# Performance work log

Hardware: AMD Instinct MI355X
Metric: run time of the kernel (lower is better)

## Reference

```python
import jax, jax.numpy as jnp
import numpy as np

N = 50000        # nodes
E = 1_600_000    # edges
F_IN = 128       # in_channels
H = 128          # hidden_dim (== F_IN so GCN weights stack)
L = 3            # num_layers
LSTM_H = 256     # lstm_hidden
OUT = 32         # output_dim
G = 64           # number of graphs in the batch


def setup_inputs() -> dict:
    key = jax.random.key(0)
    ks = jax.random.split(key, 8)
    x = jax.random.normal(ks[0], (N, F_IN), dtype=jnp.float32)
    edge_index = jax.random.randint(ks[1], (2, E), 0, N, dtype=jnp.int32)
    batch = jnp.sort(jax.random.randint(ks[2], (N,), 0, G, dtype=jnp.int32))
    # GCN layer weights (all [H,H] since F_IN == H), PyG-style glorot scale
    Wg = jax.random.normal(ks[3], (L, F_IN, H), dtype=jnp.float32) / np.sqrt(F_IN)
    bg = jnp.zeros((L, H), dtype=jnp.float32)
    # torch LSTM params, gate order (i, f, g, o)
    W_ih = jax.random.normal(ks[4], (4 * LSTM_H, H), dtype=jnp.float32) / np.sqrt(H)
    W_hh = jax.random.normal(ks[5], (4 * LSTM_H, LSTM_H), dtype=jnp.float32) / np.sqrt(LSTM_H)
    b_ih = jnp.zeros((4 * LSTM_H,), dtype=jnp.float32)
    b_hh = jnp.zeros((4 * LSTM_H,), dtype=jnp.float32)
    W_out = jax.random.normal(ks[6], (OUT, LSTM_H), dtype=jnp.float32) / np.sqrt(LSTM_H)
    b_out = jnp.zeros((OUT,), dtype=jnp.float32)
    return dict(x=x, edge_index=edge_index, batch=batch, Wg=Wg, bg=bg,
                W_ih=W_ih, W_hh=W_hh, b_ih=b_ih, b_hh=b_hh,
                W_out=W_out, b_out=b_out)


def reference(x, edge_index, batch, Wg, bg, W_ih, W_hh, b_ih, b_hh, W_out, b_out):
    n = x.shape[0]
    # PyG GCNConv gcn_norm: add self-loops, symmetric D^{-1/2}(A+I)D^{-1/2}
    loop = jnp.arange(n, dtype=edge_index.dtype)
    row = jnp.concatenate([edge_index[0], loop])  # source nodes (x_j)
    col = jnp.concatenate([edge_index[1], loop])  # target nodes (aggregate here)
    deg = jax.ops.segment_sum(jnp.ones_like(col, dtype=x.dtype), col, num_segments=n)
    dinv = jnp.where(deg > 0, jax.lax.rsqrt(deg), 0.0)
    norm = (dinv[row] * dinv[col])[:, None]  # [E+N, 1]

    h = x
    for l in range(Wg.shape[0]):
        t = h @ Wg[l]                                     # [N, H] transform first
        msg = t[row] * norm                               # gather + scale  [E+N, H]
        agg = jax.ops.segment_sum(msg, col, num_segments=n)  # scatter-add  [N, H]
        h = jax.nn.relu(agg + bg[l])

    # global_mean_pool over batch segment ids
    cnt = jax.ops.segment_sum(jnp.ones((n,), h.dtype), batch, num_segments=G)
    pooled = jax.ops.segment_sum(h, batch, num_segments=G) / jnp.maximum(cnt, 1.0)[:, None]  # [G, H]

    # single-step LSTM with zero initial state (seq_len = 1)
    h0 = jnp.zeros((G, W_hh.shape[1]), pooled.dtype)
    gates = pooled @ W_ih.T + h0 @ W_hh.T + b_ih + b_hh   # [G, 4*LSTM_H]
    i, f, g, o = jnp.split(gates, 4, axis=-1)             # torch gate order i,f,g,o
    c = jax.nn.sigmoid(i) * jnp.tanh(g)                   # c0 = 0 => forget term drops
    hn = jax.nn.sigmoid(o) * jnp.tanh(c)                  # [G, LSTM_H]

    return hn @ W_out.T + b_out                            # [G, OUT]
```

## Files before the change

kernel.cpp:

```cpp
#include <hip/hip_runtime.h>

constexpr int NN = 50000;
constexpr int NE = 1600000;
constexpr int H  = 128;
constexpr int LH = 256;
constexpr int OD = 32;
constexpr int NG = 64;

constexpr int NBKT  = (NN + 255) / 256;
constexpr int PARTE = 4096;
constexpr int NPARTB = (NE + PARTE - 1) / PARTE;
static_assert(NBKT <= 256, "single-block scan assumes NBKT <= 256");

constexpr int NCH = 8;
constexpr int CHW = 16;
constexpr int BCH = 4;
constexpr int BCW = 32;

constexpr int LSZ = 4608;

typedef __attribute__((ext_vector_type(8))) short short8v;
typedef __attribute__((ext_vector_type(4))) float f32x4;

union BF8 { uint4 u; short8v s; };

__device__ __forceinline__ unsigned short f2bf(float x) {
    unsigned int u = __float_as_uint(x);
    u = (u + 0x7FFFu + ((u >> 16) & 1u)) >> 16;
    return (unsigned short)u;
}

__global__ __launch_bounds__(256) void k_bhist(const int* __restrict__ col,
                                               int* __restrict__ bktCnt) {
    __shared__ int h[NBKT];
    int t = threadIdx.x;
    if (t < NBKT) h[t] = 0;
    __syncthreads();
    for (int i = blockIdx.x * 256 + t; i < NE; i += gridDim.x * 256)
        atomicAdd(&h[col[i] >> 8], 1);
    __syncthreads();
    if (t < NBKT && h[t] > 0) atomicAdd(&bktCnt[t], h[t]);
}

__global__ __launch_bounds__(256) void k_bscan(const int* __restrict__ bktCnt,
                                               int* __restrict__ bktBase,
                                               int* __restrict__ bktCursor) {
    __shared__ int sh[256];
    int t = threadIdx.x;
    int v = (t < NBKT) ? bktCnt[t] : 0;
    sh[t] = v;
    __syncthreads();
    for (int off = 1; off < 256; off <<= 1) {
        int add = (t >= off) ? sh[t - off] : 0;
        __syncthreads();
        sh[t] += add;
        __syncthreads();
    }
    if (t < NBKT) {
        int excl = sh[t] - v;
        bktBase[t] = excl;
        bktCursor[t] = excl;
    }
    if (t == NBKT - 1) bktBase[NBKT] = sh[t];
}

__global__ __launch_bounds__(256) void k_part(const int* __restrict__ ei,
                                              int* __restrict__ bktCursor,
                                              int* __restrict__ part) {
    __shared__ int lcur[NBKT];
    __shared__ int lbase[NBKT];
    const int t = threadIdx.x;
    const int base = blockIdx.x * PARTE;
    int pk[16], bk[16];

    if (t < NBKT) lcur[t] = 0;
    __syncthreads();
#pragma unroll
    for (int j = 0; j < 16; ++j) {
        int e = base + j * 256 + t;
        if (e < NE) {
            int sr = ei[e];
            int ds = ei[NE + e];
            pk[j] = (sr << 8) | (ds & 255);
            bk[j] = ds >> 8;
            atomicAdd(&lcur[bk[j]], 1);
        }
    }
    __syncthreads();
    if (t < NBKT) {
        int c = lcur[t];
        lbase[t] = (c > 0) ? atomicAdd(&bktCursor[t], c) : 0;
        lcur[t] = 0;
    }
    __syncthreads();
#pragma unroll
    for (int j = 0; j < 16; ++j) {
        int e = base + j * 256 + t;
        if (e < NE) {
            int r = atomicAdd(&lcur[bk[j]], 1);
            part[lbase[bk[j]] + r] = pk[j];
        }
    }
}

__global__ __launch_bounds__(256) void k_bfill(const int* __restrict__ bktBase,
                                               const int* __restrict__ part,
                                               int* __restrict__ rp,
                                               int* __restrict__ cnt,
                                               float* __restrict__ dinv,
                                               int* __restrict__ srcs) {
    __shared__ int h[256];
    __shared__ int sc[256];
    __shared__ int cur[256];
    const int b = blockIdx.x, t = threadIdx.x;
    const int lo = bktBase[b], hi = bktBase[b + 1];

    h[t] = 0;
    __syncthreads();
    for (int i = lo + t; i < hi; i += 256)
        atomicAdd(&h[part[i] & 255], 1);
    __syncthreads();
    int v = h[t];
    sc[t] = v;
    __syncthreads();
    for (int off = 1; off < 256; off <<= 1) {
        int add = (t >= off) ? sc[t - off] : 0;
        __syncthreads();
        sc[t] += add;
        __syncthreads();
    }
    int excl = sc[t] - v;
    cur[t] = lo + excl;
    int node = b * 256 + t;
    if (node < NN) {
        rp[node] = lo + excl;
        cnt[node] = v;
        dinv[node] = rsqrtf((float)v + 1.0f);
    }
    __syncthreads();
    for (int i = lo + t; i < hi; i += 256) {
        int e = part[i];
        int pos = atomicAdd(&cur[e & 255], 1);
        srcs[pos] = e >> 8;
    }
}

template <bool RELU, bool CHIN>
__global__ __launch_bounds__(256) void k_gemm(const float* __restrict__ h,
                                              const float* __restrict__ W,
                                              const float* __restrict__ dinv,
                                              unsigned short* __restrict__ tb) {
    __shared__ uint4 lw[2048];
    const int tid = threadIdx.x;

    for (int e = tid; e < 2048; e += 256) {
        const int ct = e >> 8, ks = (e >> 6) & 3, l = e & 63;
        const int col = ct * 16 + (l & 15);
        const int kb  = ks * 32 + ((l >> 4) << 3);
        const float* wp = W + (size_t)kb * H + col;
        unsigned int p0 = (unsigned)f2bf(wp[0])     | ((unsigned)f2bf(wp[H])     << 16);
        unsigned int p1 = (unsigned)f2bf(wp[2 * H]) | ((unsigned)f2bf(wp[3 * H]) << 16);
        unsigned int p2 = (unsigned)f2bf(wp[4 * H]) | ((unsigned)f2bf(wp[5 * H]) << 16);
        unsigned int p3 = (unsigned)f2bf(wp[6 * H]) | ((unsigned)f2bf(wp[7 * H]) << 16);
        lw[e] = make_uint4(p0, p1, p2, p3);
    }
    __syncthreads();

    const int wave = tid >> 6, lane = tid & 63;
    const int rowbase = blockIdx.x * 64 + wave * 16;
    const int arow  = rowbase + (lane & 15);
    const int arowc = arow < NN ? arow : NN - 1;
    const int koff  = (lane >> 4) << 3;

    f32x4 acc[8];
#pragma unroll
    for (int ct = 0; ct < 8; ++ct) acc[ct] = (f32x4){0.f, 0.f, 0.f, 0.f};

#pragma unroll
    for (int ks = 0; ks < 4; ++ks) {
        const int kb = ks * 32 + koff;
        float4 h0, h1;
        if (CHIN) {
            const float* base = h + ((size_t)(kb >> 4) * NN + arowc) * CHW + (kb & 8);
            h0 = *reinterpret_cast<const float4*>(base);
            h1 = *reinterpret_cast<const float4*>(base + 4);
        } else {
            const float* base = h + (size_t)arowc * H + kb;
            h0 = *reinterpret_cast<const float4*>(base);
            h1 = *reinterpret_cast<const float4*>(base + 4);
        }
        if (RELU) {
            h0.x = fmaxf(h0.x, 0.f); h0.y = fmaxf(h0.y, 0.f);
            h0.z = fmaxf(h0.z, 0.f); h0.w = fmaxf(h0.w, 0.f);
            h1.x = fmaxf(h1.x, 0.f); h1.y = fmaxf(h1.y, 0.f);
            h1.z = fmaxf(h1.z, 0.f); h1.w = fmaxf(h1.w, 0.f);
        }
        BF8 a;
        a.u = make_uint4(
            (unsigned)f2bf(h0.x) | ((unsigned)f2bf(h0.y) << 16),
            (unsigned)f2bf(h0.z) | ((unsigned)f2bf(h0.w) << 16),
            (unsigned)f2bf(h1.x) | ((unsigned)f2bf(h1.y) << 16),
            (unsigned)f2bf(h1.z) | ((unsigned)f2bf(h1.w) << 16));
#pragma unroll
        for (int ct = 0; ct < 8; ++ct) {
            BF8 b;
            b.u = lw[(ct * 4 + ks) * 64 + lane];
            acc[ct] = __builtin_amdgcn_mfma_f32_16x16x32_bf16(a.s, b.s, acc[ct], 0, 0, 0);
        }
    }

    const int colb = lane & 15;
    const int rrow = rowbase + ((lane >> 4) << 2);
#pragma unroll
    for (int r = 0; r < 4; ++r) {
        const int row = rrow + r;
        if (row < NN) {
            const float d = dinv[row];
#pragma unroll
            for (int ct = 0; ct < 8; ++ct) {
                const int feat = ct * 16 + colb;
                tb[((size_t)(feat >> 5) * NN + row) * BCW + (feat & 31)] =
                    f2bf(acc[ct][r] * d);
            }
        }
    }
}

__global__ __launch_bounds__(256) void k_gather(const int* __restrict__ rp,
                                                const int* __restrict__ cnt,
                                                const int* __restrict__ srcs,
                                                const float* __restrict__ dinv,
                                                const float* __restrict__ bg,
                                                const unsigned short* __restrict__ tb,
                                                float* __restrict__ agg) {
    __shared__ int lsrcs[LSZ];
    const int tid  = threadIdx.x;
    const int wv   = tid >> 6;
    const int lane = tid & 63;
    const int slot = lane >> 2;
    const int l4   = lane & 3;
    const int c    = blockIdx.x & 3;
    const int nb   = blockIdx.x >> 2;
    const int n0   = nb * 64;
    const int n    = n0 + wv * 16 + slot;

    const int eLo = rp[n0];
    int nLast = n0 + 63; if (nLast >= NN) nLast = NN - 1;
    const int eHi = rp[nLast] + cnt[nLast];
    const bool staged = (eHi - eLo) <= LSZ;

    if (staged) {
        for (int i = eLo + tid; i < eHi; i += 256)
            lsrcs[i - eLo] = srcs[i];
    }
    __syncthreads();

    if (n >= NN) return;

    const uint4* __restrict__ tb4 =
        reinterpret_cast<const uint4*>(tb) + (size_t)c * NN * 4;
    const float4 bg0 = *reinterpret_cast<const float4*>(bg + c * BCW + l4 * 8);
    const float4 bg1 = *reinterpret_cast<const float4*>(bg + c * BCW + l4 * 8 + 4);

    const int i0  = rp[n];
    const int end = i0 + cnt[n];
    float4 p = make_float4(0.f, 0.f, 0.f, 0.f);
    float4 q = make_float4(0.f, 0.f, 0.f, 0.f);

#define ACC8(v)                                                        \
    do {                                                               \
        p.x += __uint_as_float((v).x << 16);                           \
        p.y += __uint_as_float((v).x & 0xFFFF0000u);                   \
        p.z += __uint_as_float((v).y << 16);                           \
        p.w += __uint_as_float((v).y & 0xFFFF0000u);                   \
        q.x += __uint_as_float((v).z << 16);                           \
        q.y += __uint_as_float((v).z & 0xFFFF0000u);                   \
        q.z += __uint_as_float((v).w << 16);                           \
        q.w += __uint_as_float((v).w & 0xFFFF0000u);                   \
    } while (0)

    if (staged) {
        int i = i0;
        for (; i + 7 < end; i += 8) {
            int s0 = lsrcs[i     - eLo], s1 = lsrcs[i + 1 - eLo];
            int s2 = lsrcs[i + 2 - eLo], s3 = lsrcs[i + 3 - eLo];
            int s4 = lsrcs[i + 4 - eLo], s5 = lsrcs[i + 5 - eLo];
            int s6 = lsrcs[i + 6 - eLo], s7 = lsrcs[i + 7 - eLo];
            uint4 v0 = tb4[(size_t)s0 * 4 + l4];
            uint4 v1 = tb4[(size_t)s1 * 4 + l4];
            uint4 v2 = tb4[(size_t)s2 * 4 + l4];
            uint4 v3 = tb4[(size_t)s3 * 4 + l4];
            uint4 v4 = tb4[(size_t)s4 * 4 + l4];
            uint4 v5 = tb4[(size_t)s5 * 4 + l4];
            uint4 v6 = tb4[(size_t)s6 * 4 + l4];
            uint4 v7 = tb4[(size_t)s7 * 4 + l4];
            ACC8(v0); ACC8(v1); ACC8(v2); ACC8(v3);
            ACC8(v4); ACC8(v5); ACC8(v6); ACC8(v7);
        }
        for (; i < end; ++i) {
            uint4 v = tb4[(size_t)lsrcs[i - eLo] * 4 + l4];
            ACC8(v);
        }
    } else {
        int i = i0;
        for (; i + 3 < end; i += 4) {
            int s0 = srcs[i], s1 = srcs[i + 1], s2 = srcs[i + 2], s3 = srcs[i + 3];
            uint4 v0 = tb4[(size_t)s0 * 4 + l4];
            uint4 v1 = tb4[(size_t)s1 * 4 + l4];
            uint4 v2 = tb4[(size_t)s2 * 4 + l4];
            uint4 v3 = tb4[(size_t)s3 * 4 + l4];
            ACC8(v0); ACC8(v1); ACC8(v2); ACC8(v3);
        }
        for (; i < end; ++i) {
            uint4 v = tb4[(size_t)srcs[i] * 4 + l4];
            ACC8(v);
        }
    }

    uint4 sv = tb4[(size_t)n * 4 + l4];
    ACC8(sv);
#undef ACC8

    const float d = dinv[n];
    float4 o0, o1;
    o0.x = fmaf(p.x, d, bg0.x); o0.y = fmaf(p.y, d, bg0.y);
    o0.z = fmaf(p.z, d, bg0.z); o0.w = fmaf(p.w, d, bg0.w);
    o1.x = fmaf(q.x, d, bg1.x); o1.y = fmaf(q.y, d, bg1.y);
    o1.z = fmaf(q.z, d, bg1.z); o1.w = fmaf(q.w, d, bg1.w);

    const int fc = 2 * c + (l4 >> 1);
    float* dst = agg + ((size_t)fc * NN + n) * CHW + (l4 & 1) * 8;
    *reinterpret_cast<float4*>(dst)     = o0;
    *reinterpret_cast<float4*>(dst + 4) = o1;
}

__device__ __forceinline__ int lower_bound_dev(const int* __restrict__ b, int v) {
    int lo = 0, hi = NN;
    while (lo < hi) {
        int m = (lo + hi) >> 1;
        if (b[m] < v) lo = m + 1; else hi = m;
    }
    return lo;
}

__global__ __launch_bounds__(128) void k_pool(const int* __restrict__ batch,
                                              const float* __restrict__ agg,
                                              float* __restrict__ pooled,
                                              float* __restrict__ gcnt) {
    int g = blockIdx.x >> 3;
    int q = blockIdx.x & 7;
    int tid = threadIdx.x;
    int s = lower_bound_dev(batch, g);
    int e = lower_bound_dev(batch, g + 1);
    const float* __restrict__ ac = agg + (size_t)(tid >> 4) * NN * CHW + (tid & 15);
    float sum = 0.f;
    for (int n = s + q; n < e; n += 8)
        sum += fmaxf(ac[(size_t)n * CHW], 0.f);
    atomicAdd(&pooled[g * H + tid], sum);
    if (q == 0 && tid == 0) gcnt[g] = (float)(e - s);
}

__global__ __launch_bounds__(256) void k_lstm(const float* __restrict__ pooled,
                                              const float* __restrict__ gcnt,
                                              const float* __restrict__ W_ih,
                                              const float* __restrict__ b_ih,
                                              const float* __restrict__ b_hh,
                                              const float* __restrict__ W_out,
                                              const float* __restrict__ b_out,
                                              float* __restrict__ out) {
    __shared__ __align__(16) float p[H];
    __shared__ __align__(16) float hn[LH];
    int g = blockIdx.x, t = threadIdx.x;
    if (t < H) p[t] = pooled[g * H + t] / fmaxf(gcnt[g], 1.f);
    __syncthreads();

    float si = b_ih[t] + b_hh[t];
    float sg = b_ih[2 * LH + t] + b_hh[2 * LH + t];
    float so = b_ih[3 * LH + t] + b_hh[3 * LH + t];
    const float* wi = W_ih + (size_t)t * H;
    const float* wg = W_ih + (size_t)(2 * LH + t) * H;
    const float* wo = W_ih + (size_t)(3 * LH + t) * H;
    for (int k = 0; k < H; k += 4) {
        float4 pv = *reinterpret_cast<const float4*>(&p[k]);
        float4 a = *reinterpret_cast<const float4*>(wi + k);
        si += pv.x * a.x + pv.y * a.y + pv.z * a.z + pv.w * a.w;
        float4 b = *reinterpret_cast<const float4*>(wg + k);
        sg += pv.x * b.x + pv.y * b.y + pv.z * b.z + pv.w * b.w;
        float4 c = *reinterpret_cast<const float4*>(wo + k);
        so += pv.x * c.x + pv.y * c.y + pv.z * c.z + pv.w * c.w;
    }
    float ig = 1.f / (1.f + expf(-si));
    float cc = ig * tanhf(sg);
    float og = 1.f / (1.f + expf(-so));
    hn[t] = og * tanhf(cc);
    __syncthreads();

    if (t < OD) {
        float acc = b_out[t];
        const float* wr = W_out + (size_t)t * LH;
        for (int k = 0; k < LH; k += 4) {
            float4 hv = *reinterpret_cast<const float4*>(&hn[k]);
            float4 wv = *reinterpret_cast<const float4*>(wr + k);
            acc += hv.x * wv.x + hv.y * wv.y + hv.z * wv.z + hv.w * wv.w;
        }
        out[g * OD + t] = acc;
    }
}

extern "C" void kernel_launch(void* const* d_in, const int* in_sizes, int n_in,
                              void* d_out, int out_size, void* d_ws, size_t ws_size,
                              hipStream_t stream) {
    const float* x     = (const float*)d_in[0];
    const int*   ei    = (const int*)d_in[1];
    const int*   batch = (const int*)d_in[2];
    const float* Wg    = (const float*)d_in[3];
    const float* bg    = (const float*)d_in[4];
    const float* W_ih  = (const float*)d_in[5];
    const float* b_ih  = (const float*)d_in[7];
    const float* b_hh  = (const float*)d_in[8];
    const float* W_out = (const float*)d_in[9];
    const float* b_out = (const float*)d_in[10];
    float* out = (float*)d_out;

    float* ws = (float*)d_ws;
    unsigned short* tb = (unsigned short*)ws;
    float* buf1      = ws + (size_t)NN * H / 2;
    int*   part      = (int*)(buf1 + (size_t)NN * H);
    float* dinv      = (float*)(part + NE);
    float* pooled    = dinv + NN;
    float* gcnt      = pooled + NG * H;
    int*   cnt       = (int*)(gcnt + NG);
    int*   rp        = cnt + NN;
    int*   srcs      = rp + NN;
    int*   bktCnt    = srcs + NE;
    int*   bktBase   = bktCnt + NBKT;
    int*   bktCursor = bktBase + NBKT + 1;

    hipMemsetAsync(bktCnt, 0, NBKT * sizeof(int), stream);
    hipMemsetAsync(pooled, 0, (NG * H + NG) * sizeof(float), stream);

    k_bhist<<<256, 256, 0, stream>>>(ei + NE, bktCnt);
    k_bscan<<<1, 256, 0, stream>>>(bktCnt, bktBase, bktCursor);
    k_part <<<NPARTB, 256, 0, stream>>>(ei, bktCursor, part);
    k_bfill<<<NBKT, 256, 0, stream>>>(bktBase, part, rp, cnt, dinv, srcs);

    const int gemmBlocks = (NN + 63) / 64;
    const int gathBlocks = ((NN + 63) / 64) * BCH;

    k_gemm<false, false><<<gemmBlocks, 256, 0, stream>>>(x, Wg, dinv, tb);
    k_gather<<<gathBlocks, 256, 0, stream>>>(rp, cnt, srcs, dinv, bg, tb, buf1);
    k_gemm<true, true><<<gemmBlocks, 256, 0, stream>>>(buf1, Wg + H * H, dinv, tb);
    k_gather<<<gathBlocks, 256, 0, stream>>>(rp, cnt, srcs, dinv, bg + H, tb, buf1);
    k_gemm<true, true><<<gemmBlocks, 256, 0, stream>>>(buf1, Wg + 2 * H * H, dinv, tb);
    k_gather<<<gathBlocks, 256, 0, stream>>>(rp, cnt, srcs, dinv, bg + 2 * H, tb, buf1);

    k_pool<<<NG * 8, 128, 0, stream>>>(batch, buf1, pooled, gcnt);
    k_lstm<<<NG, 256, 0, stream>>>(pooled, gcnt, W_ih, b_ih, b_hh, W_out, b_out, out);
}
```

Baseline: 292.9 us.

## Store aggregated activations as bf16 and fuse mean-pool into final gather

The gather kernel now writes its output as bf16 in the 32-wide chunk layout that the next GEMM reads directly. The GEMM applies ReLU with a sign-bit mask instead of converting from fp32. This halves the intermediate write and read traffic between layers. The last gather applies ReLU and accumulates the graph pool sums in shared memory, then issues global atomics, which removes the separate pooling pass and the full fp32 activation write; node counts are recomputed in the LSTM kernel. The trade-offs are extra rounding to bf16, more atomic contention, and a barrier placed after an early return.

```diff
diff --git a/kernel.cpp b/kernel.cpp
--- a/kernel.cpp
+++ b/kernel.cpp
@@ -12,8 +12,6 @@
 constexpr int NPARTB = (NE + PARTE - 1) / PARTE;
 static_assert(NBKT <= 256, "single-block scan assumes NBKT <= 256");
 
-constexpr int NCH = 8;
-constexpr int CHW = 16;
 constexpr int BCH = 4;
 constexpr int BCW = 32;
 
@@ -146,7 +144,8 @@
 }
 
 template <bool RELU, bool CHIN>
-__global__ __launch_bounds__(256) void k_gemm(const float* __restrict__ h,
+__global__ __launch_bounds__(256) void k_gemm(const float* __restrict__ hf,
+                                              const unsigned short* __restrict__ hb,
                                               const float* __restrict__ W,
                                               const float* __restrict__ dinv,
                                               unsigned short* __restrict__ tb) {
@@ -178,29 +177,34 @@
 
 #pragma unroll
     for (int ks = 0; ks < 4; ++ks) {
-        const int kb = ks * 32 + koff;
-        float4 h0, h1;
+        BF8 a;
         if (CHIN) {
-            const float* base = h + ((size_t)(kb >> 4) * NN + arowc) * CHW + (kb & 8);
-            h0 = *reinterpret_cast<const float4*>(base);
-            h1 = *reinterpret_cast<const float4*>(base + 4);
+            a.u = *reinterpret_cast<const uint4*>(
+                hb + ((size_t)ks * NN + arowc) * BCW + koff);
+            if (RELU) {
+                unsigned int m;
+                m = ((a.u.x >> 15) & 0x00010001u) * 0xFFFFu; a.u.x &= ~m;
+                m = ((a.u.y >> 15) & 0x00010001u) * 0xFFFFu; a.u.y &= ~m;
+                m = ((a.u.z >> 15) & 0x00010001u) * 0xFFFFu; a.u.z &= ~m;
+                m = ((a.u.w >> 15) & 0x00010001u) * 0xFFFFu; a.u.w &= ~m;
+            }
         } else {
-            const float* base = h + (size_t)arowc * H + kb;
-            h0 = *reinterpret_cast<const float4*>(base);
-            h1 = *reinterpret_cast<const float4*>(base + 4);
-        }
-        if (RELU) {
-            h0.x = fmaxf(h0.x, 0.f); h0.y = fmaxf(h0.y, 0.f);
-            h0.z = fmaxf(h0.z, 0.f); h0.w = fmaxf(h0.w, 0.f);
-            h1.x = fmaxf(h1.x, 0.f); h1.y = fmaxf(h1.y, 0.f);
-            h1.z = fmaxf(h1.z, 0.f); h1.w = fmaxf(h1.w, 0.f);
-        }
-        BF8 a;
-        a.u = make_uint4(
-            (unsigned)f2bf(h0.x) | ((unsigned)f2bf(h0.y) << 16),
-            (unsigned)f2bf(h0.z) | ((unsigned)f2bf(h0.w) << 16),
-            (unsigned)f2bf(h1.x) | ((unsigned)f2bf(h1.y) << 16),
-            (unsigned)f2bf(h1.z) | ((unsigned)f2bf(h1.w) << 16));
+            const int kb = ks * 32 + koff;
+            const float* base = hf + (size_t)arowc * H + kb;
+            float4 h0 = *reinterpret_cast<const float4*>(base);
+            float4 h1 = *reinterpret_cast<const float4*>(base + 4);
+            if (RELU) {
+                h0.x = fmaxf(h0.x, 0.f); h0.y = fmaxf(h0.y, 0.f);
+                h0.z = fmaxf(h0.z, 0.f); h0.w = fmaxf(h0.w, 0.f);
+                h1.x = fmaxf(h1.x, 0.f); h1.y = fmaxf(h1.y, 0.f);
+                h1.z = fmaxf(h1.z, 0.f); h1.w = fmaxf(h1.w, 0.f);
+            }
+            a.u = make_uint4(
+                (unsigned)f2bf(h0.x) | ((unsigned)f2bf(h0.y) << 16),
+                (unsigned)f2bf(h0.z) | ((unsigned)f2bf(h0.w) << 16),
+                (unsigned)f2bf(h1.x) | ((unsigned)f2bf(h1.y) << 16),
+                (unsigned)f2bf(h1.z) | ((unsigned)f2bf(h1.w) << 16));
+        }
 #pragma unroll
         for (int ct = 0; ct < 8; ++ct) {
             BF8 b;
@@ -226,13 +230,16 @@
     }
 }
 
+template <int POOL>
 __global__ __launch_bounds__(256) void k_gather(const int* __restrict__ rp,
                                                 const int* __restrict__ cnt,
                                                 const int* __restrict__ srcs,
                                                 const float* __restrict__ dinv,
                                                 const float* __restrict__ bg,
                                                 const unsigned short* __restrict__ tb,
-                                                float* __restrict__ agg) {
+                                                unsigned short* __restrict__ aggb,
+                                                const int* __restrict__ batch,
+                                                float* __restrict__ pooled) {
     __shared__ int lsrcs[LSZ];
     const int tid  = threadIdx.x;
     const int wv   = tid >> 6;
@@ -252,6 +259,17 @@
     if (staged) {
         for (int i = eLo + tid; i < eHi; i += 256)
             lsrcs[i - eLo] = srcs[i];
+    }
+
+#if 1
+    __shared__ float psum[4][32];
+#endif
+    int g0 = 0;
+    bool bigspan = false;
+    if (POOL) {
+        if (tid < 128) psum[tid >> 5][tid & 31] = 0.f;
+        g0 = batch[n0];
+        bigspan = (batch[nLast] - g0) > 3;
     }
     __syncthreads();
 
@@ -328,10 +346,44 @@
     o1.x = fmaf(q.x, d, bg1.x); o1.y = fmaf(q.y, d, bg1.y);
     o1.z = fmaf(q.z, d, bg1.z); o1.w = fmaf(q.w, d, bg1.w);
 
-    const int fc = 2 * c + (l4 >> 1);
-    float* dst = agg + ((size_t)fc * NN + n) * CHW + (l4 & 1) * 8;
-    *reinterpret_cast<float4*>(dst)     = o0;
-    *reinterpret_cast<float4*>(dst + 4) = o1;
+    if (POOL == 0) {
+        uint4 u;
+        u.x = (unsigned)f2bf(o0.x) | ((unsigned)f2bf(o0.y) << 16);
+        u.y = (unsigned)f2bf(o0.z) | ((unsigned)f2bf(o0.w) << 16);
+        u.z = (unsigned)f2bf(o1.x) | ((unsigned)f2bf(o1.y) << 16);
+        u.w = (unsigned)f2bf(o1.z) | ((unsigned)f2bf(o1.w) << 16);
+        *reinterpret_cast<uint4*>(aggb + ((size_t)c * NN + n) * BCW + l4 * 8) = u;
+    } else {
+        o0.x = fmaxf(o0.x, 0.f); o0.y = fmaxf(o0.y, 0.f);
+        o0.z = fmaxf(o0.z, 0.f); o0.w = fmaxf(o0.w, 0.f);
+        o1.x = fmaxf(o1.x, 0.f); o1.y = fmaxf(o1.y, 0.f);
+        o1.z = fmaxf(o1.z, 0.f); o1.w = fmaxf(o1.w, 0.f);
+        if (bigspan) {
+            float* dst = pooled + (size_t)batch[n] * H + c * BCW + l4 * 8;
+            atomicAdd(dst + 0, o0.x); atomicAdd(dst + 1, o0.y);
+            atomicAdd(dst + 2, o0.z); atomicAdd(dst + 3, o0.w);
+            atomicAdd(dst + 4, o1.x); atomicAdd(dst + 5, o1.y);
+            atomicAdd(dst + 6, o1.z); atomicAdd(dst + 7, o1.w);
+        } else {
+            const int gi = batch[n] - g0;
+            float* ps = &psum[gi][l4 * 8];
+            atomicAdd(ps + 0, o0.x); atomicAdd(ps + 1, o0.y);
+            atomicAdd(ps + 2, o0.z); atomicAdd(ps + 3, o0.w);
+            atomicAdd(ps + 4, o1.x); atomicAdd(ps + 5, o1.y);
+            atomicAdd(ps + 6, o1.z); atomicAdd(ps + 7, o1.w);
+            __syncthreads();
+            if (tid < 64) {
+#pragma unroll
+                for (int k = 0; k < 2; ++k) {
+                    int idx = tid + k * 64;
+                    int gi2 = idx >> 5, f = idx & 31;
+                    float v = psum[gi2][f];
+                    if (v != 0.f)
+                        atomicAdd(&pooled[(size_t)(g0 + gi2) * H + c * BCW + f], v);
+                }
+            }
+        }
+    }
 }
 
 __device__ __forceinline__ int lower_bound_dev(const int* __restrict__ b, int v) {
@@ -343,25 +395,8 @@
     return lo;
 }
 
-__global__ __launch_bounds__(128) void k_pool(const int* __restrict__ batch,
-                                              const float* __restrict__ agg,
-                                              float* __restrict__ pooled,
-                                              float* __restrict__ gcnt) {
-    int g = blockIdx.x >> 3;
-    int q = blockIdx.x & 7;
-    int tid = threadIdx.x;
-    int s = lower_bound_dev(batch, g);
-    int e = lower_bound_dev(batch, g + 1);
-    const float* __restrict__ ac = agg + (size_t)(tid >> 4) * NN * CHW + (tid & 15);
-    float sum = 0.f;
-    for (int n = s + q; n < e; n += 8)
-        sum += fmaxf(ac[(size_t)n * CHW], 0.f);
-    atomicAdd(&pooled[g * H + tid], sum);
-    if (q == 0 && tid == 0) gcnt[g] = (float)(e - s);
-}
-
 __global__ __launch_bounds__(256) void k_lstm(const float* __restrict__ pooled,
-                                              const float* __restrict__ gcnt,
+                                              const int* __restrict__ batch,
                                               const float* __restrict__ W_ih,
                                               const float* __restrict__ b_ih,
                                               const float* __restrict__ b_hh,
@@ -371,7 +406,11 @@
     __shared__ __align__(16) float p[H];
     __shared__ __align__(16) float hn[LH];
     int g = blockIdx.x, t = threadIdx.x;
-    if (t < H) p[t] = pooled[g * H + t] / fmaxf(gcnt[g], 1.f);
+    if (t < H) {
+        int s = lower_bound_dev(batch, g);
+        int e = lower_bound_dev(batch, g + 1);
+        p[t] = pooled[g * H + t] / fmaxf((float)(e - s), 1.f);
+    }
     __syncthreads();
 
     float si = b_ih[t] + b_hh[t];
@@ -422,14 +461,12 @@
     const float* b_out = (const float*)d_in[10];
     float* out = (float*)d_out;
 
-    float* ws = (float*)d_ws;
-    unsigned short* tb = (unsigned short*)ws;
-    float* buf1      = ws + (size_t)NN * H / 2;
-    int*   part      = (int*)(buf1 + (size_t)NN * H);
+    unsigned short* tb   = (unsigned short*)d_ws;
+    unsigned short* aggb = tb + (size_t)NN * H;
+    int*   part      = (int*)(aggb + (size_t)NN * H);
     float* dinv      = (float*)(part + NE);
     float* pooled    = dinv + NN;
-    float* gcnt      = pooled + NG * H;
-    int*   cnt       = (int*)(gcnt + NG);
+    int*   cnt       = (int*)(pooled + NG * H);
     int*   rp        = cnt + NN;
     int*   srcs      = rp + NN;
     int*   bktCnt    = srcs + NE;
@@ -437,7 +474,7 @@
     int*   bktCursor = bktBase + NBKT + 1;
 
     hipMemsetAsync(bktCnt, 0, NBKT * sizeof(int), stream);
-    hipMemsetAsync(pooled, 0, (NG * H + NG) * sizeof(float), stream);
+    hipMemsetAsync(pooled, 0, NG * H * sizeof(float), stream);
 
     k_bhist<<<256, 256, 0, stream>>>(ei + NE, bktCnt);
     k_bscan<<<1, 256, 0, stream>>>(bktCnt, bktBase, bktCursor);
@@ -447,13 +484,12 @@
     const int gemmBlocks = (NN + 63) / 64;
     const int gathBlocks = ((NN + 63) / 64) * BCH;
 
-    k_gemm<false, false><<<gemmBlocks, 256, 0, stream>>>(x, Wg, dinv, tb);
-    k_gather<<<gathBlocks, 256, 0, stream>>>(rp, cnt, srcs, dinv, bg, tb, buf1);
-    k_gemm<true, true><<<gemmBlocks, 256, 0, stream>>>(buf1, Wg + H * H, dinv, tb);
-    k_gather<<<gathBlocks, 256, 0, stream>>>(rp, cnt, srcs, dinv, bg + H, tb, buf1);
-    k_gemm<true, true><<<gemmBlocks, 256, 0, stream>>>(buf1, Wg + 2 * H * H, dinv, tb);
-    k_gather<<<gathBlocks, 256, 0, stream>>>(rp, cnt, srcs, dinv, bg + 2 * H, tb, buf1);
-
-    k_pool<<<NG * 8, 128, 0, stream>>>(batch, buf1, pooled, gcnt);
-    k_lstm<<<NG, 256, 0, stream>>>(pooled, gcnt, W_ih, b_ih, b_hh, W_out, b_out, out);
-}
+    k_gemm<false, false><<<gemmBlocks, 256, 0, stream>>>(x, nullptr, Wg, dinv, tb);
+    k_gather<0><<<gathBlocks, 256, 0, stream>>>(rp, cnt, srcs, dinv, bg, tb, aggb, batch, pooled);
+    k_gemm<true, true><<<gemmBlocks, 256, 0, stream>>>(nullptr, aggb, Wg + H * H, dinv, tb);
+    k_gather<0><<<gathBlocks, 256, 0, stream>>>(rp, cnt, srcs, dinv, bg + H, tb, aggb, batch, pooled);
+    k_gemm<true, true><<<gemmBlocks, 256, 0, stream>>>(nullptr, aggb, Wg + 2 * H * H, dinv, tb);
+    k_gather<1><<<gathBlocks, 256, 0, stream>>>(rp, cnt, srcs, dinv, bg + 2 * H, tb, nullptr, batch, pooled);
+
+    k_lstm<<<NG, 256, 0, stream>>>(pooled, batch, W_ih, b_ih, b_hh, W_out, b_out, out);
+}
```

Result: faster. 280.1 us (-4.4%).
